# Optimization experiments

Hardware: AMD Instinct MI355X
Metric: run time of the kernel (lower is better)

The kernel has to match this reference:

```python
import jax, jax.numpy as jnp
import numpy as np

N = 100000   # nodes
E = 100000   # hyperedges
M = 1600000  # incidences
IN_C = 128
HID = 128
OUT_C = 64
L = 2
EPS = 1e-5


def _layer_norm(x, g, b):
    m = jnp.mean(x, axis=-1, keepdims=True)
    v = jnp.mean((x - m) ** 2, axis=-1, keepdims=True)
    return (x - m) * jax.lax.rsqrt(v + EPS) * g + b


def setup_inputs() -> dict:
    key = jax.random.key(0)
    ks = jax.random.split(key, 16)
    s_in = 1.0 / np.sqrt(IN_C)
    s_h = 1.0 / np.sqrt(HID)
    return {
        "x": jax.random.normal(ks[0], (N, IN_C), jnp.float32),
        "x_e": jax.random.normal(ks[1], (E, IN_C), jnp.float32),
        "edge_index": jax.random.randint(ks[2], (2, M), 0, N, jnp.int32),
        "in_norm_g": jnp.ones((IN_C,), jnp.float32),
        "in_norm_b": jnp.zeros((IN_C,), jnp.float32),
        "in_proj_W": jax.random.normal(ks[3], (IN_C, HID), jnp.float32) * s_in,
        "in_proj_b": jnp.zeros((HID,), jnp.float32),
        "norm_g": jnp.ones((L, HID), jnp.float32),
        "norm_b": jnp.zeros((L, HID), jnp.float32),
        "conv_W": jax.random.normal(ks[4], (L, HID, HID), jnp.float32) * s_h,
        "conv_b": jnp.zeros((L, HID), jnp.float32),
        "lin_W": jax.random.normal(ks[5], (HID, OUT_C), jnp.float32) * s_h,
        "lin_b": jnp.zeros((OUT_C,), jnp.float32),
    }


def reference(x, x_e, edge_index, in_norm_g, in_norm_b, in_proj_W, in_proj_b,
              norm_g, norm_b, conv_W, conv_b, lin_W, lin_b):
    src, dst = edge_index[0], edge_index[1]  # node ids, hyperedge ids
    h = _layer_norm(x, in_norm_g, in_norm_b)
    h = jax.nn.leaky_relu(h @ in_proj_W + in_proj_b)  # dropout = identity (eval)

    # HypergraphConv degree normalizers (hyperedge_weight = 1)
    ones = jnp.ones((M,), h.dtype)
    degD = jax.ops.segment_sum(ones, src, num_segments=N)
    D = jnp.where(degD > 0, 1.0 / degD, 0.0)          # [N]
    degB = jax.ops.segment_sum(ones, dst, num_segments=E)
    B = jnp.where(degB > 0, 1.0 / degB, 0.0)          # [E]

    for i in range(L):
        hn = _layer_norm(h, norm_g[i], norm_b[i])
        xw = hn @ conv_W[i]                            # [N, HID]
        # node -> hyperedge: sum_j B[e] * xw[j]
        he = jax.ops.segment_sum(B[dst][:, None] * xw[src], dst, num_segments=E)
        # hyperedge -> node: sum_e D[n] * he[e]
        h2 = jax.ops.segment_sum(D[src][:, None] * he[dst], src, num_segments=N)
        h = jax.nn.leaky_relu(h2 + conv_b[i])

    # MinAggregation: segment-min of gathered node features per hyperedge
    agg = jax.ops.segment_min(h[src], dst, num_segments=E)  # [E, HID]
    return agg @ lin_W + lin_b                              # [E, OUT_C]
```

## Files before the change

kernel.cpp:

```cpp
#include <hip/hip_runtime.h>

#define NN 100000
#define NE 100000
#define MI 1600000
#define HID 128
#define OUTC 64
#define LSLOPE 0.01f
#define EPSV 1e-5f
#define ADJ_STRIDE 48
#define BUILD_PASSES 6
#define BUILD_WIN ((NN + BUILD_PASSES - 1) / BUILD_PASSES)

typedef unsigned short us;
typedef __attribute__((ext_vector_type(4))) unsigned short us4;
typedef __attribute__((ext_vector_type(8))) short short8;
typedef __attribute__((ext_vector_type(16))) float f32x16;

__device__ __forceinline__ float bf2f(us h) {
    return __uint_as_float(((unsigned)h) << 16);
}
__device__ __forceinline__ us f2bf(float f) {
    unsigned u = __float_as_uint(f);
    return (us)((u + 0x7FFFu + ((u >> 16) & 1u)) >> 16);
}

__global__ void build_win_kernel(const int* __restrict__ ei,
                                 int* __restrict__ cntE, int* __restrict__ cntN,
                                 int* __restrict__ adjE, int* __restrict__ adjN,
                                 int lo, int hi) {
    int m = blockIdx.x * blockDim.x + threadIdx.x;
    if (m >= MI) return;
    int s = ei[m], d = ei[MI + m];
    if (d >= lo && d < hi) {
        int p = atomicAdd(&cntE[d], 1);
        if (p < ADJ_STRIDE) adjE[d * ADJ_STRIDE + p] = s;
    }
    if (s >= lo && s < hi) {
        int p = atomicAdd(&cntN[s], 1);
        if (p < ADJ_STRIDE) adjN[s * ADJ_STRIDE + p] = d;
    }
}

__global__ void recip2_kernel(const int* __restrict__ cntE, const int* __restrict__ cntN,
                              float* __restrict__ B, float* __restrict__ D) {
    int i = blockIdx.x * blockDim.x + threadIdx.x;
    if (i < NE) {
        int d = cntE[i]; B[i] = d > 0 ? 1.0f / (float)d : 0.0f;
    } else if (i < NE + NN) {
        int j = i - NE;
        int d = cntN[j]; D[j] = d > 0 ? 1.0f / (float)d : 0.0f;
    }
}

__global__ void wprep_kernel(const float* __restrict__ in_W, const float* __restrict__ conv_W,
                             const float* __restrict__ lin_W,
                             us* __restrict__ wt_in, us* __restrict__ wt_c0,
                             us* __restrict__ wt_c1, us* __restrict__ wt_lin) {
    int idx = blockIdx.x * blockDim.x + threadIdx.x;
    if (idx < 49152) {
        int mat = idx >> 14, r = idx & 16383;
        const float* src = mat == 0 ? in_W : (mat == 1 ? conv_W : conv_W + 16384);
        us* dst = mat == 0 ? wt_in : (mat == 1 ? wt_c0 : wt_c1);
        int n = r >> 7, k = r & 127;
        dst[r] = f2bf(src[k * 128 + n]);
    } else if (idx < 57344) {
        int r = idx - 49152;
        int n = r >> 7, k = r & 127;
        float v = lin_W[k * 64 + n];
        us h = f2bf(v);
        wt_lin[r] = h;
        wt_lin[8192 + r] = f2bf(v - bf2f(h));
    }
}

template <int MODE>
__global__ __launch_bounds__(256) void gather_kernel(
    const int* __restrict__ cnt, const int* __restrict__ adj,
    const us* __restrict__ src, const float* __restrict__ scale,
    const float* __restrict__ bias, us* __restrict__ dst, int R)
{
    int g = threadIdx.x >> 5;
    int lane = threadIdx.x & 31;
    int r = blockIdx.x * 8 + g;
    if (r >= R) return;
    int n = cnt[r]; n = n < ADJ_STRIDE ? n : ADJ_STRIDE;
    const int* arow = adj + (size_t)r * ADJ_STRIDE;
    float ax, ay, az, aw;
    if (MODE == 2) { ax = ay = az = aw = INFINITY; }
    else           { ax = ay = az = aw = 0.f; }
    const us* base = src + lane * 4;
    int j = 0;
    for (; j + 7 < n; j += 8) {
        us4 v0 = *(const us4*)(base + (size_t)arow[j]     * HID);
        us4 v1 = *(const us4*)(base + (size_t)arow[j + 1] * HID);
        us4 v2 = *(const us4*)(base + (size_t)arow[j + 2] * HID);
        us4 v3 = *(const us4*)(base + (size_t)arow[j + 3] * HID);
        us4 v4 = *(const us4*)(base + (size_t)arow[j + 4] * HID);
        us4 v5 = *(const us4*)(base + (size_t)arow[j + 5] * HID);
        us4 v6 = *(const us4*)(base + (size_t)arow[j + 6] * HID);
        us4 v7 = *(const us4*)(base + (size_t)arow[j + 7] * HID);
        if (MODE == 2) {
            ax = fminf(ax, fminf(fminf(fminf(bf2f(v0.x), bf2f(v1.x)), fminf(bf2f(v2.x), bf2f(v3.x))),
                                 fminf(fminf(bf2f(v4.x), bf2f(v5.x)), fminf(bf2f(v6.x), bf2f(v7.x)))));
            ay = fminf(ay, fminf(fminf(fminf(bf2f(v0.y), bf2f(v1.y)), fminf(bf2f(v2.y), bf2f(v3.y))),
                                 fminf(fminf(bf2f(v4.y), bf2f(v5.y)), fminf(bf2f(v6.y), bf2f(v7.y)))));
            az = fminf(az, fminf(fminf(fminf(bf2f(v0.z), bf2f(v1.z)), fminf(bf2f(v2.z), bf2f(v3.z))),
                                 fminf(fminf(bf2f(v4.z), bf2f(v5.z)), fminf(bf2f(v6.z), bf2f(v7.z)))));
            aw = fminf(aw, fminf(fminf(fminf(bf2f(v0.w), bf2f(v1.w)), fminf(bf2f(v2.w), bf2f(v3.w))),
                                 fminf(fminf(bf2f(v4.w), bf2f(v5.w)), fminf(bf2f(v6.w), bf2f(v7.w)))));
        } else {
            ax += ((bf2f(v0.x) + bf2f(v1.x)) + (bf2f(v2.x) + bf2f(v3.x)))
                + ((bf2f(v4.x) + bf2f(v5.x)) + (bf2f(v6.x) + bf2f(v7.x)));
            ay += ((bf2f(v0.y) + bf2f(v1.y)) + (bf2f(v2.y) + bf2f(v3.y)))
                + ((bf2f(v4.y) + bf2f(v5.y)) + (bf2f(v6.y) + bf2f(v7.y)));
            az += ((bf2f(v0.z) + bf2f(v1.z)) + (bf2f(v2.z) + bf2f(v3.z)))
                + ((bf2f(v4.z) + bf2f(v5.z)) + (bf2f(v6.z) + bf2f(v7.z)));
            aw += ((bf2f(v0.w) + bf2f(v1.w)) + (bf2f(v2.w) + bf2f(v3.w)))
                + ((bf2f(v4.w) + bf2f(v5.w)) + (bf2f(v6.w) + bf2f(v7.w)));
        }
    }
    for (; j + 1 < n; j += 2) {
        us4 v0 = *(const us4*)(base + (size_t)arow[j]     * HID);
        us4 v1 = *(const us4*)(base + (size_t)arow[j + 1] * HID);
        if (MODE == 2) {
            ax = fminf(ax, fminf(bf2f(v0.x), bf2f(v1.x)));
            ay = fminf(ay, fminf(bf2f(v0.y), bf2f(v1.y)));
            az = fminf(az, fminf(bf2f(v0.z), bf2f(v1.z)));
            aw = fminf(aw, fminf(bf2f(v0.w), bf2f(v1.w)));
        } else {
            ax += bf2f(v0.x) + bf2f(v1.x);
            ay += bf2f(v0.y) + bf2f(v1.y);
            az += bf2f(v0.z) + bf2f(v1.z);
            aw += bf2f(v0.w) + bf2f(v1.w);
        }
    }
    if (j < n) {
        us4 v0 = *(const us4*)(base + (size_t)arow[j] * HID);
        if (MODE == 2) {
            ax = fminf(ax, bf2f(v0.x)); ay = fminf(ay, bf2f(v0.y));
            az = fminf(az, bf2f(v0.z)); aw = fminf(aw, bf2f(v0.w));
        } else {
            ax += bf2f(v0.x); ay += bf2f(v0.y); az += bf2f(v0.z); aw += bf2f(v0.w);
        }
    }
    if (MODE == 0) {
        float s = scale[r];
        ax *= s; ay *= s; az *= s; aw *= s;
    } else if (MODE == 1) {
        float s = scale[r];
        float4 b = *(const float4*)(bias + lane * 4);
        float x;
        x = s * ax + b.x; ax = x > 0.f ? x : LSLOPE * x;
        x = s * ay + b.y; ay = x > 0.f ? x : LSLOPE * x;
        x = s * az + b.z; az = x > 0.f ? x : LSLOPE * x;
        x = s * aw + b.w; aw = x > 0.f ? x : LSLOPE * x;
    }
    us4 o;
    o.x = f2bf(ax); o.y = f2bf(ay); o.z = f2bf(az); o.w = f2bf(aw);
    *(us4*)(dst + (size_t)r * HID + lane * 4) = o;
}

template <int NC, bool ABF16, bool OBF16, bool SPLIT>
__global__ __launch_bounds__(512) void mfma_gemm_kernel(
    const void* __restrict__ Av, const float* __restrict__ ln_g, const float* __restrict__ ln_b,
    const us* __restrict__ WT, const float* __restrict__ bias,
    void* __restrict__ outv, int R, int flags)
{
    constexpr int SA = 136;
    constexpr int NW = (SPLIT ? 2 : 1) * NC;
    constexpr int CT = NC / 64;
    __shared__ us As[128 * SA];
    __shared__ us Ws[NW * SA];
    __shared__ float red_s[512];
    __shared__ float red_q[512];
    __shared__ float r_mean[128];
    __shared__ float r_rstd[128];

    const int t = threadIdx.x;
    const int row0 = blockIdx.x * 128;

    constexpr int WUS4 = NW * 128 / 4;
    #pragma unroll
    for (int i = t; i < WUS4; i += 512) {
        us4 w = ((const us4*)WT)[i];
        int nrow = i >> 5, k4 = i & 31;
        *(us4*)(Ws + nrow * SA + k4 * 4) = w;
    }

    {
        const int r = t >> 2, sub = t & 3;
        const int gr = row0 + r;
        float v[32];
        if (gr < R) {
            if (ABF16) {
                const us* ap = (const us*)Av + (size_t)gr * 128 + sub * 32;
                #pragma unroll
                for (int j4 = 0; j4 < 8; ++j4) {
                    us4 x4 = *(const us4*)(ap + j4 * 4);
                    v[j4 * 4 + 0] = bf2f(x4.x); v[j4 * 4 + 1] = bf2f(x4.y);
                    v[j4 * 4 + 2] = bf2f(x4.z); v[j4 * 4 + 3] = bf2f(x4.w);
                }
            } else {
                const float* ap = (const float*)Av + (size_t)gr * 128 + sub * 32;
                #pragma unroll
                for (int j4 = 0; j4 < 8; ++j4) {
                    float4 f4 = *(const float4*)(ap + j4 * 4);
                    v[j4 * 4 + 0] = f4.x; v[j4 * 4 + 1] = f4.y;
                    v[j4 * 4 + 2] = f4.z; v[j4 * 4 + 3] = f4.w;
                }
            }
        } else {
            #pragma unroll
            for (int j = 0; j < 32; ++j) v[j] = 0.f;
        }
        if (flags & 1) {
            float s = 0.f, q = 0.f;
            #pragma unroll
            for (int j = 0; j < 32; ++j) { s += v[j]; q += v[j] * v[j]; }
            red_s[t] = s; red_q[t] = q;
            __syncthreads();
            if (t < 128) {
                float ss = red_s[t * 4] + red_s[t * 4 + 1] + red_s[t * 4 + 2] + red_s[t * 4 + 3];
                float qq = red_q[t * 4] + red_q[t * 4 + 1] + red_q[t * 4 + 2] + red_q[t * 4 + 3];
                float mu = ss * (1.0f / 128.0f);
                float var = qq * (1.0f / 128.0f) - mu * mu;
                r_mean[t] = mu;
                r_rstd[t] = rsqrtf(var + EPSV);
            }
            __syncthreads();
            float mu = r_mean[r], rs = r_rstd[r];
            #pragma unroll
            for (int j4 = 0; j4 < 8; ++j4) {
                float4 g4 = *(const float4*)(ln_g + sub * 32 + j4 * 4);
                float4 b4 = *(const float4*)(ln_b + sub * 32 + j4 * 4);
                v[j4 * 4 + 0] = (v[j4 * 4 + 0] - mu) * rs * g4.x + b4.x;
                v[j4 * 4 + 1] = (v[j4 * 4 + 1] - mu) * rs * g4.y + b4.y;
                v[j4 * 4 + 2] = (v[j4 * 4 + 2] - mu) * rs * g4.z + b4.z;
                v[j4 * 4 + 3] = (v[j4 * 4 + 3] - mu) * rs * g4.w + b4.w;
            }
        }
        #pragma unroll
        for (int j4 = 0; j4 < 8; ++j4) {
            us4 o;
            o.x = f2bf(v[j4 * 4 + 0]); o.y = f2bf(v[j4 * 4 + 1]);
            o.z = f2bf(v[j4 * 4 + 2]); o.w = f2bf(v[j4 * 4 + 3]);
            *(us4*)(As + r * SA + sub * 32 + j4 * 4) = o;
        }
    }
    __syncthreads();

    const int lane = t & 63;
    const int wave = t >> 6;
    const int wr = (wave & 3) * 32;
    const int wc = (wave >> 2) * (NC / 2);
    const int m = lane & 31;
    const int half = lane >> 5;
    const us* a_base = As + (wr + m) * SA + half * 8;

    f32x16 acc[CT];
    #pragma unroll
    for (int ct = 0; ct < CT; ++ct) acc[ct] = (f32x16)(0.0f);

    #pragma unroll
    for (int ks = 0; ks < 8; ++ks) {
        short8 a = *(const short8*)(a_base + ks * 16);
        #pragma unroll
        for (int ct = 0; ct < CT; ++ct) {
            const us* b_base = Ws + (wc + ct * 32 + m) * SA + half * 8 + ks * 16;
            short8 b = *(const short8*)b_base;
            acc[ct] = __builtin_amdgcn_mfma_f32_32x32x16_bf16(a, b, acc[ct], 0, 0, 0);
            if (SPLIT) {
                short8 bl = *(const short8*)(b_base + (size_t)NC * SA);
                acc[ct] = __builtin_amdgcn_mfma_f32_32x32x16_bf16(a, bl, acc[ct], 0, 0, 0);
            }
        }
    }

    #pragma unroll
    for (int ct = 0; ct < CT; ++ct) {
        int gc = wc + ct * 32 + m;
        float bv = bias ? bias[gc] : 0.f;
        #pragma unroll
        for (int reg = 0; reg < 16; ++reg) {
            int rloc = (reg & 3) + 8 * (reg >> 2) + 4 * half;
            int gr = row0 + wr + rloc;
            if (gr < R) {
                float y = acc[ct][reg] + bv;
                if (flags & 4) y = y > 0.f ? y : LSLOPE * y;
                if (OBF16) ((us*)outv)[(size_t)gr * NC + gc] = f2bf(y);
                else       ((float*)outv)[(size_t)gr * NC + gc] = y;
            }
        }
    }
}

extern "C" void kernel_launch(void* const* d_in, const int* in_sizes, int n_in,
                              void* d_out, int out_size, void* d_ws, size_t ws_size,
                              hipStream_t stream) {
    const float* x      = (const float*)d_in[0];
    const int*   ei     = (const int*)d_in[2];
    const float* in_g   = (const float*)d_in[3];
    const float* in_b   = (const float*)d_in[4];
    const float* in_W   = (const float*)d_in[5];
    const float* in_pb  = (const float*)d_in[6];
    const float* norm_g = (const float*)d_in[7];
    const float* norm_b = (const float*)d_in[8];
    const float* conv_W = (const float*)d_in[9];
    const float* conv_b = (const float*)d_in[10];
    const float* lin_W  = (const float*)d_in[11];
    const float* lin_b  = (const float*)d_in[12];
    float* out = (float*)d_out;

    us* h_bf   = (us*)d_ws;
    us* xw_bf  = h_bf  + (size_t)NN * HID;
    us* he_bf  = xw_bf + (size_t)NN * HID;
    us* agg_bf = he_bf + (size_t)NE * HID;
    float* D    = (float*)(agg_bf + (size_t)NE * HID);
    float* B    = D + NN;
    int* cntE   = (int*)(B + NE);
    int* cntN   = cntE + NE;
    int* adjE   = cntN + NN;
    int* adjN   = adjE + (size_t)NE * ADJ_STRIDE;
    us* wt_in  = (us*)(adjN + (size_t)NN * ADJ_STRIDE);
    us* wt_c0  = wt_in + 128 * 128;
    us* wt_c1  = wt_c0 + 128 * 128;
    us* wt_lin = wt_c1 + 128 * 128;

    hipMemsetAsync(cntE, 0, (size_t)(NN + NE) * sizeof(int), stream);
    for (int p = 0; p < BUILD_PASSES; ++p) {
        int lo = p * BUILD_WIN;
        int hi = lo + BUILD_WIN < NN ? lo + BUILD_WIN : NN;
        build_win_kernel<<<(MI + 255) / 256, 256, 0, stream>>>(ei, cntE, cntN, adjE, adjN, lo, hi);
    }
    recip2_kernel<<<(NN + NE + 255) / 256, 256, 0, stream>>>(cntE, cntN, B, D);

    wprep_kernel<<<(57344 + 255) / 256, 256, 0, stream>>>(
        in_W, conv_W, lin_W, wt_in, wt_c0, wt_c1, wt_lin);

    mfma_gemm_kernel<HID, false, true, false><<<(NN + 127) / 128, 512, 0, stream>>>(
        x, in_g, in_b, wt_in, in_pb, h_bf, NN, 1 | 4);

    for (int i = 0; i < 2; ++i) {
        mfma_gemm_kernel<HID, true, true, false><<<(NN + 127) / 128, 512, 0, stream>>>(
            h_bf, norm_g + i * HID, norm_b + i * HID, i ? wt_c1 : wt_c0,
            nullptr, xw_bf, NN, 1);
        gather_kernel<0><<<(NE + 7) / 8, 256, 0, stream>>>(cntE, adjE, xw_bf, B, nullptr, he_bf, NE);
        gather_kernel<1><<<(NN + 7) / 8, 256, 0, stream>>>(cntN, adjN, he_bf, D, conv_b + i * HID, h_bf, NN);
    }

    gather_kernel<2><<<(NE + 7) / 8, 256, 0, stream>>>(cntE, adjE, h_bf, nullptr, nullptr, agg_bf, NE);

    mfma_gemm_kernel<OUTC, true, false, true><<<(NE + 127) / 128, 512, 0, stream>>>(
        agg_bf, nullptr, nullptr, wt_lin, lin_b, out, NE, 0);
}
```

Measured before the change: 757.8 us.

## Fuse adjacency build passes into one cooperative kernel with grid syncs

Replaces the multi-launch windowed adjacency build, the reciprocal-degree kernel and the weight-prep kernel with a single cooperative kernel. Each thread loads its edge indices into registers once and loops over the windows, with grid.sync between passes. The number of windows goes from 6 to 10, which shrinks the atomic working set per pass. This removes repeated edge-index reads and launch overheads, at the cost of grid-wide barriers and a dependence on all 2048 blocks being co-resident.

New measurement: 2.993 ms. 295% more time.

```diff
diff --git a/kernel.cpp b/kernel.cpp
--- a/kernel.cpp
+++ b/kernel.cpp
@@ -1,4 +1,7 @@
 #include <hip/hip_runtime.h>
+#include <hip/hip_cooperative_groups.h>
+
+namespace cg = cooperative_groups;
 
 #define NN 100000
 #define NE 100000
@@ -8,8 +11,11 @@
 #define LSLOPE 0.01f
 #define EPSV 1e-5f
 #define ADJ_STRIDE 48
-#define BUILD_PASSES 6
+#define BUILD_PASSES 10
 #define BUILD_WIN ((NN + BUILD_PASSES - 1) / BUILD_PASSES)
+#define COOP_BLOCKS 2048
+#define COOP_THREADS (COOP_BLOCKS * 256)
+#define EPT 4
 
 typedef unsigned short us;
 typedef __attribute__((ext_vector_type(4))) unsigned short us4;
@@ -24,52 +30,65 @@
     return (us)((u + 0x7FFFu + ((u >> 16) & 1u)) >> 16);
 }
 
-__global__ void build_win_kernel(const int* __restrict__ ei,
-                                 int* __restrict__ cntE, int* __restrict__ cntN,
-                                 int* __restrict__ adjE, int* __restrict__ adjN,
-                                 int lo, int hi) {
-    int m = blockIdx.x * blockDim.x + threadIdx.x;
-    if (m >= MI) return;
-    int s = ei[m], d = ei[MI + m];
-    if (d >= lo && d < hi) {
-        int p = atomicAdd(&cntE[d], 1);
-        if (p < ADJ_STRIDE) adjE[d * ADJ_STRIDE + p] = s;
-    }
-    if (s >= lo && s < hi) {
-        int p = atomicAdd(&cntN[s], 1);
-        if (p < ADJ_STRIDE) adjN[s * ADJ_STRIDE + p] = d;
-    }
-}
-
-__global__ void recip2_kernel(const int* __restrict__ cntE, const int* __restrict__ cntN,
-                              float* __restrict__ B, float* __restrict__ D) {
-    int i = blockIdx.x * blockDim.x + threadIdx.x;
+__global__ void build_coop_kernel(const int* __restrict__ ei,
+                                  int* __restrict__ cntE, int* __restrict__ cntN,
+                                  int* __restrict__ adjE, int* __restrict__ adjN,
+                                  float* __restrict__ B, float* __restrict__ D,
+                                  const float* __restrict__ in_W,
+                                  const float* __restrict__ conv_W,
+                                  const float* __restrict__ lin_W,
+                                  us* __restrict__ wt_in, us* __restrict__ wt_c0,
+                                  us* __restrict__ wt_c1, us* __restrict__ wt_lin) {
+    cg::grid_group grid = cg::this_grid();
+    const int tid = blockIdx.x * 256 + threadIdx.x;
+
+    int se[EPT], de[EPT];
+    int ne = 0;
+    #pragma unroll
+    for (int k = 0; k < EPT; ++k) {
+        int m = tid + k * COOP_THREADS;
+        if (m < MI) { se[ne] = ei[m]; de[ne] = ei[MI + m]; ++ne; }
+    }
+
+    for (int p = 0; p < BUILD_PASSES; ++p) {
+        int lo = p * BUILD_WIN;
+        int hi = lo + BUILD_WIN < NN ? lo + BUILD_WIN : NN;
+        for (int i = 0; i < ne; ++i) {
+            int s = se[i], d = de[i];
+            if (d >= lo && d < hi) {
+                int q = atomicAdd(&cntE[d], 1);
+                if (q < ADJ_STRIDE) adjE[d * ADJ_STRIDE + q] = s;
+            }
+            if (s >= lo && s < hi) {
+                int q = atomicAdd(&cntN[s], 1);
+                if (q < ADJ_STRIDE) adjN[s * ADJ_STRIDE + q] = d;
+            }
+        }
+        grid.sync();
+    }
+
+    int i = tid;
     if (i < NE) {
         int d = cntE[i]; B[i] = d > 0 ? 1.0f / (float)d : 0.0f;
     } else if (i < NE + NN) {
         int j = i - NE;
         int d = cntN[j]; D[j] = d > 0 ? 1.0f / (float)d : 0.0f;
-    }
-}
-
-__global__ void wprep_kernel(const float* __restrict__ in_W, const float* __restrict__ conv_W,
-                             const float* __restrict__ lin_W,
-                             us* __restrict__ wt_in, us* __restrict__ wt_c0,
-                             us* __restrict__ wt_c1, us* __restrict__ wt_lin) {
-    int idx = blockIdx.x * blockDim.x + threadIdx.x;
-    if (idx < 49152) {
-        int mat = idx >> 14, r = idx & 16383;
-        const float* src = mat == 0 ? in_W : (mat == 1 ? conv_W : conv_W + 16384);
-        us* dst = mat == 0 ? wt_in : (mat == 1 ? wt_c0 : wt_c1);
-        int n = r >> 7, k = r & 127;
-        dst[r] = f2bf(src[k * 128 + n]);
-    } else if (idx < 57344) {
-        int r = idx - 49152;
-        int n = r >> 7, k = r & 127;
-        float v = lin_W[k * 64 + n];
-        us h = f2bf(v);
-        wt_lin[r] = h;
-        wt_lin[8192 + r] = f2bf(v - bf2f(h));
+    } else {
+        int idx = i - (NE + NN);
+        if (idx < 49152) {
+            int mat = idx >> 14, r = idx & 16383;
+            const float* src = mat == 0 ? in_W : (mat == 1 ? conv_W : conv_W + 16384);
+            us* dst = mat == 0 ? wt_in : (mat == 1 ? wt_c0 : wt_c1);
+            int n = r >> 7, k = r & 127;
+            dst[r] = f2bf(src[k * 128 + n]);
+        } else if (idx < 57344) {
+            int r = idx - 49152;
+            int n = r >> 7, k = r & 127;
+            float v = lin_W[k * 64 + n];
+            us h = f2bf(v);
+            wt_lin[r] = h;
+            wt_lin[8192 + r] = f2bf(v - bf2f(h));
+        }
     }
 }
 
@@ -327,15 +346,15 @@
     us* wt_lin = wt_c1 + 128 * 128;
 
     hipMemsetAsync(cntE, 0, (size_t)(NN + NE) * sizeof(int), stream);
-    for (int p = 0; p < BUILD_PASSES; ++p) {
-        int lo = p * BUILD_WIN;
-        int hi = lo + BUILD_WIN < NN ? lo + BUILD_WIN : NN;
-        build_win_kernel<<<(MI + 255) / 256, 256, 0, stream>>>(ei, cntE, cntN, adjE, adjN, lo, hi);
-    }
-    recip2_kernel<<<(NN + NE + 255) / 256, 256, 0, stream>>>(cntE, cntN, B, D);
-
-    wprep_kernel<<<(57344 + 255) / 256, 256, 0, stream>>>(
-        in_W, conv_W, lin_W, wt_in, wt_c0, wt_c1, wt_lin);
+    {
+        void* args[] = {
+            (void*)&ei, (void*)&cntE, (void*)&cntN, (void*)&adjE, (void*)&adjN,
+            (void*)&B, (void*)&D, (void*)&in_W, (void*)&conv_W, (void*)&lin_W,
+            (void*)&wt_in, (void*)&wt_c0, (void*)&wt_c1, (void*)&wt_lin
+        };
+        hipLaunchCooperativeKernel((const void*)build_coop_kernel,
+                                   dim3(COOP_BLOCKS), dim3(256), args, 0, stream);
+    }
 
     mfma_gemm_kernel<HID, false, true, false><<<(NN + 127) / 128, 512, 0, stream>>>(
         x, in_g, in_b, wt_in, in_pb, h_bf, NN, 1 | 4);
```
